# Performance work log

Measured on AMD Instinct MI355X. Metric: run time of the kernel, lower is better.

## Reference

```python
import jax, jax.numpy as jnp
import numpy as np

N = 50000
E = 800000
D = 256
EPS = 1e-5  # BatchNorm eps


def _gcn_conv(x, W, b, row, col):
    # PyG GCNConv: h = x @ W; add self-loops; sym-normalize; scatter-add; + bias
    h = x @ W  # [N, D]
    deg = jnp.zeros((N,), x.dtype).at[col].add(jnp.ones((row.shape[0],), x.dtype))
    dinv = jax.lax.rsqrt(deg)  # deg >= 1 thanks to self-loops
    norm = dinv[row] * dinv[col]  # [E+N]
    msg = h[row] * norm[:, None]  # gather + scale, [E+N, D]
    out = jnp.zeros_like(h).at[col].add(msg)  # scatter-aggregate
    return out + b


def _bn(x, gamma, beta):
    # BatchNorm1d in training mode: batch statistics over nodes
    m = jnp.mean(x, axis=0)
    v = jnp.var(x, axis=0)
    return (x - m) * jax.lax.rsqrt(v + EPS) * gamma + beta


def setup_inputs() -> dict:
    key = jax.random.key(0)
    ks = jax.random.split(key, 4)
    x = jax.random.normal(ks[0], (N, D), dtype=jnp.float32)
    edge_index = jax.random.randint(ks[1], (2, E), 0, N, dtype=jnp.int64)
    s = 1.0 / np.sqrt(D)
    W1 = jax.random.uniform(ks[2], (D, D), jnp.float32, -s, s)
    W2 = jax.random.uniform(ks[3], (D, D), jnp.float32, -s, s)
    z = jnp.zeros((D,), jnp.float32)
    o = jnp.ones((D,), jnp.float32)
    return {"x": x, "edge_index": edge_index,
            "W1": W1, "b1": z, "g1": o, "be1": z,
            "W2": W2, "b2": z, "g2": o, "be2": z}


def reference(x, edge_index, W1, b1, g1, be1, W2, b2, g2, be2):
    loops = jnp.arange(N, dtype=edge_index.dtype)
    row = jnp.concatenate([edge_index[0], loops])  # sources
    col = jnp.concatenate([edge_index[1], loops])  # targets
    # layer 1: GCNConv -> BN -> ReLU (dropout is identity in eval)
    h = _gcn_conv(x, W1, b1, row, col)
    h = jax.nn.relu(_bn(h, g1, be1))
    # layer 2
    h = _gcn_conv(h, W2, b2, row, col)
    h = jax.nn.relu(_bn(h, g2, be2))
    return h
```

## Files before the change

### kernel.cpp

```cpp
#include <hip/hip_runtime.h>
#include <cstdint>
#include <cstddef>

constexpr int N = 50000;
constexpr int E = 800000;
constexpr int D = 256;
constexpr float EPS = 1e-5f;
constexpr int NB = (N + 255) / 256;
constexpr int BN_BLOCKS = 512;
constexpr int GB = (N + 63) / 64;

typedef __attribute__((ext_vector_type(8))) short short8;
typedef __attribute__((ext_vector_type(4))) float f32x4;

__device__ __forceinline__ unsigned short f2bf(float f) {
  union { float f; unsigned u; } c; c.f = f;
  unsigned u = c.u;
  u += 0x7fff + ((u >> 16) & 1);
  return (unsigned short)(u >> 16);
}
__device__ __forceinline__ float bf2f(unsigned short h) {
  union { unsigned u; float f; } c; c.u = ((unsigned)h) << 16;
  return c.f;
}

__global__ void k_detect(const void* __restrict__ ei, int* __restrict__ flag) {
  int t = threadIdx.x;
  const int* p = (const int*)ei;
  int nz = 0;
  for (int i = 2 * t + 1; i < 2048; i += 128) nz |= (p[i] != 0);
  unsigned long long b = __ballot(nz != 0);
  if (t == 0) *flag = (b == 0ULL) ? 1 : 0;
}

__device__ __forceinline__ int edge_at(const void* ei, int is64, long long pos) {
  if (is64) return (int)((const long long*)ei)[pos];
  return ((const int*)ei)[pos];
}

__global__ void k_count(const void* __restrict__ ei, const int* __restrict__ flag,
                        int* __restrict__ degc) {
  int e = blockIdx.x * 256 + threadIdx.x;
  if (e >= E) return;
  int is64 = *flag;
  int c = edge_at(ei, is64, (long long)E + e);
  atomicAdd(&degc[c], 1);
}

__global__ void k_scan_partial(const int* __restrict__ degc, int* __restrict__ bsum,
                               float* __restrict__ dinv) {
  __shared__ int sd[256];
  int t = threadIdx.x;
  int i = blockIdx.x * 256 + t;
  int dv = (i < N) ? degc[i] : 0;
  if (i < N) dinv[i] = rsqrtf((float)(dv + 1));
  int v = (i < N) ? (dv + 1) : 0;
  sd[t] = v;
  __syncthreads();
  for (int s = 128; s > 0; s >>= 1) {
    if (t < s) sd[t] += sd[t + s];
    __syncthreads();
  }
  if (t == 0) bsum[blockIdx.x] = sd[0];
}

__global__ void k_scan_block(int* __restrict__ bsum) {
  __shared__ int sd[256];
  int t = threadIdx.x;
  int v = (t < NB) ? bsum[t] : 0;
  sd[t] = v;
  __syncthreads();
  for (int off = 1; off < 256; off <<= 1) {
    int x = (t >= off) ? sd[t - off] : 0;
    __syncthreads();
    sd[t] += x;
    __syncthreads();
  }
  if (t < NB) bsum[t] = sd[t] - v;
}

__global__ void k_scan_final(const int* __restrict__ degc, const int* __restrict__ bsum,
                             const float* __restrict__ dinv, int* __restrict__ offs,
                             int* __restrict__ curs, int2* __restrict__ epair) {
  __shared__ int sd[256];
  int t = threadIdx.x;
  int i = blockIdx.x * 256 + t;
  int v = (i < N) ? (degc[i] + 1) : 0;
  sd[t] = v;
  __syncthreads();
  for (int off = 1; off < 256; off <<= 1) {
    int x = (t >= off) ? sd[t - off] : 0;
    __syncthreads();
    sd[t] += x;
    __syncthreads();
  }
  if (i < N) {
    int o = bsum[blockIdx.x] + sd[t] - v;
    offs[i] = o;
    curs[i] = o + 1;
    float d = dinv[i];
    epair[o] = make_int2(i, __float_as_int(d * d));
  }
  if (i == N - 1) offs[N] = bsum[blockIdx.x] + sd[t];
}

__global__ void k_fill_edges(const void* __restrict__ ei, const int* __restrict__ flag,
                             const float* __restrict__ dinv, int* __restrict__ curs,
                             int2* __restrict__ epair) {
  int e = blockIdx.x * 256 + threadIdx.x;
  if (e >= E) return;
  int is64 = *flag;
  int r = edge_at(ei, is64, e);
  int c = edge_at(ei, is64, (long long)E + e);
  int p = atomicAdd(&curs[c], 1);
  epair[p] = make_int2(r, __float_as_int(dinv[r] * dinv[c]));
}

__global__ void k_wfrag(const float* __restrict__ W, unsigned short* __restrict__ Wf) {
  int tile = blockIdx.x;
  int lane = threadIdx.x;
  int kstep = tile >> 4, wn = tile & 15;
  int kbase = kstep * 32 + (lane >> 4) * 8;
  int col = wn * 16 + (lane & 15);
  short8 v;
#pragma unroll
  for (int j = 0; j < 8; ++j)
    v[j] = (short)f2bf(W[(size_t)(kbase + j) * 256 + col]);
  *(short8*)&Wf[(((size_t)tile) * 64 + lane) * 8] = v;
}

template <bool A_BF16, bool FUSE_BN>
__global__ __launch_bounds__(256) void k_gemm(const void* __restrict__ Ap,
                                              const unsigned short* __restrict__ Wf,
                                              unsigned short* __restrict__ C,
                                              const float* __restrict__ sc,
                                              const float* __restrict__ sh) {
  __shared__ unsigned short As[64][264];
  int t = threadIdx.x;
  int lane = t & 63;
  int w = t >> 6;
  int row0 = blockIdx.x * 64;
  int l16 = lane & 15, lk = lane >> 4;

  f32x4 acc[4][4];
#pragma unroll
  for (int i = 0; i < 4; ++i)
#pragma unroll
    for (int j = 0; j < 4; ++j) acc[i][j] = (f32x4){0.f, 0.f, 0.f, 0.f};

  int arow = t >> 2;
  int ak0 = (t & 3) * 8;
  int gr = row0 + arow;
  bool inb = (gr < N);

#pragma unroll
  for (int ks = 0; ks < 8; ++ks) {
    int kc = ks * 32 + ak0;
    float f[8] = {0.f, 0.f, 0.f, 0.f, 0.f, 0.f, 0.f, 0.f};
    if (inb) {
      if (A_BF16) {
        const unsigned short* A = (const unsigned short*)Ap;
        short8 v = *(const short8*)&A[(size_t)gr * 256 + kc];
#pragma unroll
        for (int j = 0; j < 8; ++j) f[j] = bf2f((unsigned short)v[j]);
      } else {
        const float* A = (const float*)Ap;
        float4 f0 = *(const float4*)&A[(size_t)gr * 256 + kc];
        float4 f1 = *(const float4*)&A[(size_t)gr * 256 + kc + 4];
        f[0] = f0.x; f[1] = f0.y; f[2] = f0.z; f[3] = f0.w;
        f[4] = f1.x; f[5] = f1.y; f[6] = f1.z; f[7] = f1.w;
      }
    }
    if (FUSE_BN) {
#pragma unroll
      for (int j = 0; j < 8; ++j)
        f[j] = fmaxf(fmaf(f[j], sc[kc + j], sh[kc + j]), 0.f);
    }
    ushort4 u0 = {f2bf(f[0]), f2bf(f[1]), f2bf(f[2]), f2bf(f[3])};
    ushort4 u1 = {f2bf(f[4]), f2bf(f[5]), f2bf(f[6]), f2bf(f[7])};
    *(ushort4*)&As[arow][kc] = u0;
    *(ushort4*)&As[arow][kc + 4] = u1;
  }
  __syncthreads();

#pragma unroll
  for (int ks = 0; ks < 8; ++ks) {
    short8 af[4];
#pragma unroll
    for (int mf = 0; mf < 4; ++mf)
      af[mf] = *(const short8*)&As[mf * 16 + l16][ks * 32 + lk * 8];
#pragma unroll
    for (int nf = 0; nf < 4; ++nf) {
      short8 bf = *(const short8*)&Wf[(((size_t)ks * 16 + w * 4 + nf) * 64 + lane) * 8];
#pragma unroll
      for (int mf = 0; mf < 4; ++mf)
        acc[mf][nf] = __builtin_amdgcn_mfma_f32_16x16x32_bf16(af[mf], bf, acc[mf][nf], 0, 0, 0);
    }
  }
  __syncthreads();

  unsigned short(*Cs)[264] = As;
#pragma unroll
  for (int mf = 0; mf < 4; ++mf)
#pragma unroll
    for (int nf = 0; nf < 4; ++nf)
#pragma unroll
      for (int r = 0; r < 4; ++r)
        Cs[mf * 16 + lk * 4 + r][w * 64 + nf * 16 + l16] = f2bf(acc[mf][nf][r]);
  __syncthreads();
#pragma unroll
  for (int it = 0; it < 8; ++it) {
    int r = it * 8 + (t >> 5);
    int gr2 = row0 + r;
    if (gr2 < N)
      *(short8*)&C[(size_t)gr2 * 256 + (t & 31) * 8] = *(const short8*)&Cs[r][(t & 31) * 8];
  }
}

__global__ __launch_bounds__(256) void k_agg(const unsigned short* __restrict__ h,
                                             const int* __restrict__ offs,
                                             const int2* __restrict__ epair,
                                             const float* __restrict__ bias,
                                             unsigned short* __restrict__ outp) {
  int nd = blockIdx.x * 4 + (threadIdx.x >> 6);
  if (nd >= N) return;
  int node = __builtin_amdgcn_readfirstlane(nd);
  int lane = threadIdx.x & 63;
  int e = offs[node];
  int end = offs[node + 1];
  float a0 = 0.f, a1 = 0.f, a2 = 0.f, a3 = 0.f;

#define ACC4(v, wgt)                                            \
  do {                                                          \
    a0 = fmaf(wgt, bf2f((unsigned short)((v).x & 0xffff)), a0); \
    a1 = fmaf(wgt, bf2f((unsigned short)((v).x >> 16)), a1);    \
    a2 = fmaf(wgt, bf2f((unsigned short)((v).y & 0xffff)), a2); \
    a3 = fmaf(wgt, bf2f((unsigned short)((v).y >> 16)), a3);    \
  } while (0)

  for (; e + 8 <= end; e += 8) {
    int2 p0 = epair[e + 0], p1 = epair[e + 1], p2 = epair[e + 2], p3 = epair[e + 3];
    int2 p4 = epair[e + 4], p5 = epair[e + 5], p6 = epair[e + 6], p7 = epair[e + 7];
    uint2 v0 = *(const uint2*)&h[(size_t)p0.x * 256 + lane * 4];
    uint2 v1 = *(const uint2*)&h[(size_t)p1.x * 256 + lane * 4];
    uint2 v2 = *(const uint2*)&h[(size_t)p2.x * 256 + lane * 4];
    uint2 v3 = *(const uint2*)&h[(size_t)p3.x * 256 + lane * 4];
    uint2 v4 = *(const uint2*)&h[(size_t)p4.x * 256 + lane * 4];
    uint2 v5 = *(const uint2*)&h[(size_t)p5.x * 256 + lane * 4];
    uint2 v6 = *(const uint2*)&h[(size_t)p6.x * 256 + lane * 4];
    uint2 v7 = *(const uint2*)&h[(size_t)p7.x * 256 + lane * 4];
    ACC4(v0, __int_as_float(p0.y));
    ACC4(v1, __int_as_float(p1.y));
    ACC4(v2, __int_as_float(p2.y));
    ACC4(v3, __int_as_float(p3.y));
    ACC4(v4, __int_as_float(p4.y));
    ACC4(v5, __int_as_float(p5.y));
    ACC4(v6, __int_as_float(p6.y));
    ACC4(v7, __int_as_float(p7.y));
  }
  for (; e < end; ++e) {
    int2 p = epair[e];
    uint2 v = *(const uint2*)&h[(size_t)p.x * 256 + lane * 4];
    ACC4(v, __int_as_float(p.y));
  }
#undef ACC4

  float4 bb = ((const float4*)bias)[lane];
  a0 += bb.x; a1 += bb.y; a2 += bb.z; a3 += bb.w;
  ushort4 o = {f2bf(a0), f2bf(a1), f2bf(a2), f2bf(a3)};
  *(ushort4*)&outp[(size_t)nd * 256 + lane * 4] = o;
}

__global__ __launch_bounds__(256) void k_bnpart(const unsigned short* __restrict__ xp,
                                                float* __restrict__ partial) {
  int t = threadIdx.x;
  int lane = t & 63;
  int sub = t >> 6;
  float sx = 0, sy = 0, sz = 0, sw = 0;
  float qx = 0, qy = 0, qz = 0, qw = 0;
  for (int r = blockIdx.x * 4 + sub; r < N; r += gridDim.x * 4) {
    uint2 u = *(const uint2*)&xp[(size_t)r * 256 + lane * 4];
    float vx = bf2f((unsigned short)(u.x & 0xffff));
    float vy = bf2f((unsigned short)(u.x >> 16));
    float vz = bf2f((unsigned short)(u.y & 0xffff));
    float vw = bf2f((unsigned short)(u.y >> 16));
    sx += vx; sy += vy; sz += vz; sw += vw;
    qx = fmaf(vx, vx, qx); qy = fmaf(vy, vy, qy);
    qz = fmaf(vz, vz, qz); qw = fmaf(vw, vw, qw);
  }
  __shared__ float4 ps[256];
  __shared__ float4 pq[256];
  ps[t] = {sx, sy, sz, sw};
  pq[t] = {qx, qy, qz, qw};
  __syncthreads();
  float* pout = partial + (size_t)blockIdx.x * 512;
  if (t < 64) {
    float4 a = ps[t], b = ps[64 + t], c = ps[128 + t], d = ps[192 + t];
    float4 o = {a.x + b.x + c.x + d.x, a.y + b.y + c.y + d.y,
                a.z + b.z + c.z + d.z, a.w + b.w + c.w + d.w};
    ((float4*)pout)[t] = o;
  } else if (t < 128) {
    int l = t - 64;
    float4 a = pq[l], b = pq[64 + l], c = pq[128 + l], d = pq[192 + l];
    float4 o = {a.x + b.x + c.x + d.x, a.y + b.y + c.y + d.y,
                a.z + b.z + c.z + d.z, a.w + b.w + c.w + d.w};
    ((float4*)(pout + 256))[l] = o;
  }
}

__global__ __launch_bounds__(256) void k_bnred(const float* __restrict__ partial,
                                               float* __restrict__ bnsum,
                                               float* __restrict__ bnsq) {
  int t = threadIdx.x;
  float s = 0.f, q = 0.f;
  int b0 = blockIdx.x * (BN_BLOCKS / 16);
  for (int b = b0; b < b0 + BN_BLOCKS / 16; ++b) {
    s += partial[(size_t)b * 512 + t];
    q += partial[(size_t)b * 512 + 256 + t];
  }
  atomicAdd(&bnsum[t], s);
  atomicAdd(&bnsq[t], q);
}

__global__ void k_bnfinal(const float* __restrict__ bnsum, const float* __restrict__ bnsq,
                          const float* __restrict__ g, const float* __restrict__ be,
                          float* __restrict__ sc, float* __restrict__ sh) {
  int t = threadIdx.x;
  const float inv = 1.f / (float)N;
  float m = bnsum[t] * inv;
  float v = bnsq[t] * inv - m * m;
  float s = rsqrtf(v + EPS) * g[t];
  sc[t] = s;
  sh[t] = be[t] - m * s;
}

__global__ __launch_bounds__(256) void k_bnapply(const unsigned short* __restrict__ in,
                                                 float* __restrict__ outp,
                                                 const float* __restrict__ sc,
                                                 const float* __restrict__ sh) {
  int t = threadIdx.x;
  int lane = t & 63;
  int sub = t >> 6;
  float4 s4 = ((const float4*)sc)[lane];
  float4 h4 = ((const float4*)sh)[lane];
  for (int r = blockIdx.x * 4 + sub; r < N; r += gridDim.x * 4) {
    uint2 u = *(const uint2*)&in[(size_t)r * 256 + lane * 4];
    float4 v;
    v.x = fmaxf(fmaf(bf2f((unsigned short)(u.x & 0xffff)), s4.x, h4.x), 0.f);
    v.y = fmaxf(fmaf(bf2f((unsigned short)(u.x >> 16)), s4.y, h4.y), 0.f);
    v.z = fmaxf(fmaf(bf2f((unsigned short)(u.y & 0xffff)), s4.z, h4.z), 0.f);
    v.w = fmaxf(fmaf(bf2f((unsigned short)(u.y >> 16)), s4.w, h4.w), 0.f);
    *(float4*)&outp[(size_t)r * 256 + lane * 4] = v;
  }
}

extern "C" void kernel_launch(void* const* d_in, const int* in_sizes, int n_in,
                              void* d_out, int out_size, void* d_ws, size_t ws_size,
                              hipStream_t stream) {
  const float* x  = (const float*)d_in[0];
  const void*  ei = d_in[1];
  const float* W1 = (const float*)d_in[2];
  const float* b1 = (const float*)d_in[3];
  const float* g1 = (const float*)d_in[4];
  const float* be1 = (const float*)d_in[5];
  const float* W2 = (const float*)d_in[6];
  const float* b2 = (const float*)d_in[7];
  const float* g2 = (const float*)d_in[8];
  const float* be2 = (const float*)d_in[9];
  float* out = (float*)d_out;

  char* base = (char*)d_ws;
  size_t off = 0;
  unsigned short* hbuf = (unsigned short*)(base + off); off += (size_t)N * D * 2;
  unsigned short* abuf = (unsigned short*)(base + off); off += (size_t)N * D * 2;
  unsigned short* Wf1 = (unsigned short*)(base + off);  off += (size_t)D * D * 2;
  unsigned short* Wf2 = (unsigned short*)(base + off);  off += (size_t)D * D * 2;
  int*   degc = (int*)(base + off);   off += (size_t)N * 4;
  float* dinv = (float*)(base + off); off += (size_t)N * 4;
  int*   offs = (int*)(base + off);   off += (size_t)(N + 4) * 4;
  int*   curs = (int*)(base + off);   off += (size_t)N * 4;
  int2*  epair = (int2*)(base + off); off += (size_t)(E + N) * 8;
  float* partial = (float*)(base + off); off += (size_t)BN_BLOCKS * 512 * 4;
  float* bnsum = (float*)(base + off); off += (size_t)D * 4;
  float* bnsq  = (float*)(base + off); off += (size_t)D * 4;
  float* sc1 = (float*)(base + off);  off += (size_t)D * 4;
  float* sh1 = (float*)(base + off);  off += (size_t)D * 4;
  float* sc2 = (float*)(base + off);  off += (size_t)D * 4;
  float* sh2 = (float*)(base + off);  off += (size_t)D * 4;
  int*   bsum = (int*)(base + off);   off += 256 * 4;
  int*   flag = (int*)(base + off);   off += 16;

  k_wfrag<<<128, 64, 0, stream>>>(W1, Wf1);
  k_wfrag<<<128, 64, 0, stream>>>(W2, Wf2);

  hipMemsetAsync(degc, 0, (size_t)N * 4, stream);
  k_detect<<<1, 64, 0, stream>>>(ei, flag);
  k_count<<<(E + 255) / 256, 256, 0, stream>>>(ei, flag, degc);
  k_scan_partial<<<NB, 256, 0, stream>>>(degc, bsum, dinv);
  k_scan_block<<<1, 256, 0, stream>>>(bsum);
  k_scan_final<<<NB, 256, 0, stream>>>(degc, bsum, dinv, offs, curs, epair);
  k_fill_edges<<<(E + 255) / 256, 256, 0, stream>>>(ei, flag, dinv, curs, epair);

  k_gemm<false, false><<<GB, 256, 0, stream>>>(x, Wf1, hbuf, nullptr, nullptr);
  k_agg<<<(N + 3) / 4, 256, 0, stream>>>(hbuf, offs, epair, b1, abuf);
  hipMemsetAsync(bnsum, 0, 2 * (size_t)D * 4, stream);
  k_bnpart<<<BN_BLOCKS, 256, 0, stream>>>(abuf, partial);
  k_bnred<<<16, 256, 0, stream>>>(partial, bnsum, bnsq);
  k_bnfinal<<<1, 256, 0, stream>>>(bnsum, bnsq, g1, be1, sc1, sh1);

  k_gemm<true, true><<<GB, 256, 0, stream>>>(abuf, Wf2, hbuf, sc1, sh1);
  k_agg<<<(N + 3) / 4, 256, 0, stream>>>(hbuf, offs, epair, b2, abuf);
  hipMemsetAsync(bnsum, 0, 2 * (size_t)D * 4, stream);
  k_bnpart<<<BN_BLOCKS, 256, 0, stream>>>(abuf, partial);
  k_bnred<<<16, 256, 0, stream>>>(partial, bnsum, bnsq);
  k_bnfinal<<<1, 256, 0, stream>>>(bnsum, bnsq, g2, be2, sc2, sh2);
  k_bnapply<<<512, 256, 0, stream>>>(abuf, out, sc2, sh2);
}
```

Before: 315.4 us.

## Store features in 32-column panels and split aggregation per panel for cache locality

Intermediate bf16 feature matrices are stored as eight column panels of 32 features, so each panel (about 3.2 MB) can stay resident in cache during the gather. Aggregation is split into 8 chunk blocks per node group, with four lane groups working on different edges and reduced by shuffles. The edge list drops the precomputed weights and stores only source indices, computing dinv[src]*dinv[dst] on the fly. The two weight-fragment launches and the memsets are also merged. The cost is 8x more aggregation blocks, each re-reading offsets and indices, plus smaller 4-byte gathers per lane.

```diff
diff --git a/kernel.cpp b/kernel.cpp
--- a/kernel.cpp
+++ b/kernel.cpp
@@ -9,6 +9,8 @@
 constexpr int NB = (N + 255) / 256;
 constexpr int BN_BLOCKS = 512;
 constexpr int GB = (N + 63) / 64;
+constexpr int PANEL = 32;
+constexpr size_t PSTRIDE = (size_t)N * PANEL;
 
 typedef __attribute__((ext_vector_type(8))) short short8;
 typedef __attribute__((ext_vector_type(4))) float f32x4;
@@ -80,8 +82,8 @@
 }
 
 __global__ void k_scan_final(const int* __restrict__ degc, const int* __restrict__ bsum,
-                             const float* __restrict__ dinv, int* __restrict__ offs,
-                             int* __restrict__ curs, int2* __restrict__ epair) {
+                             int* __restrict__ offs, int* __restrict__ curs,
+                             int* __restrict__ esrc) {
   __shared__ int sd[256];
   int t = threadIdx.x;
   int i = blockIdx.x * 256 + t;
@@ -98,26 +100,28 @@
     int o = bsum[blockIdx.x] + sd[t] - v;
     offs[i] = o;
     curs[i] = o + 1;
-    float d = dinv[i];
-    epair[o] = make_int2(i, __float_as_int(d * d));
+    esrc[o] = i;
   }
   if (i == N - 1) offs[N] = bsum[blockIdx.x] + sd[t];
 }
 
 __global__ void k_fill_edges(const void* __restrict__ ei, const int* __restrict__ flag,
-                             const float* __restrict__ dinv, int* __restrict__ curs,
-                             int2* __restrict__ epair) {
+                             int* __restrict__ curs, int* __restrict__ esrc) {
   int e = blockIdx.x * 256 + threadIdx.x;
   if (e >= E) return;
   int is64 = *flag;
   int r = edge_at(ei, is64, e);
   int c = edge_at(ei, is64, (long long)E + e);
   int p = atomicAdd(&curs[c], 1);
-  epair[p] = make_int2(r, __float_as_int(dinv[r] * dinv[c]));
-}
-
-__global__ void k_wfrag(const float* __restrict__ W, unsigned short* __restrict__ Wf) {
-  int tile = blockIdx.x;
+  esrc[p] = r;
+}
+
+__global__ void k_wfrag(const float* __restrict__ W1, const float* __restrict__ W2,
+                        unsigned short* __restrict__ Wf1, unsigned short* __restrict__ Wf2) {
+  int b = blockIdx.x;
+  const float* W = (b < 128) ? W1 : W2;
+  unsigned short* Wf = (b < 128) ? Wf1 : Wf2;
+  int tile = b & 127;
   int lane = threadIdx.x;
   int kstep = tile >> 4, wn = tile & 15;
   int kbase = kstep * 32 + (lane >> 4) * 8;
@@ -160,7 +164,7 @@
     if (inb) {
       if (A_BF16) {
         const unsigned short* A = (const unsigned short*)Ap;
-        short8 v = *(const short8*)&A[(size_t)gr * 256 + kc];
+        short8 v = *(const short8*)&A[(size_t)ks * PSTRIDE + (size_t)gr * 32 + ak0];
 #pragma unroll
         for (int j = 0; j < 8; ++j) f[j] = bf2f((unsigned short)v[j]);
       } else {
@@ -212,63 +216,68 @@
   for (int it = 0; it < 8; ++it) {
     int r = it * 8 + (t >> 5);
     int gr2 = row0 + r;
+    int cb = t & 31;
+    int ch = cb >> 2;
+    int ic = (cb & 3) * 8;
     if (gr2 < N)
-      *(short8*)&C[(size_t)gr2 * 256 + (t & 31) * 8] = *(const short8*)&Cs[r][(t & 31) * 8];
+      *(short8*)&C[(size_t)ch * PSTRIDE + (size_t)gr2 * 32 + ic] =
+          *(const short8*)&Cs[r][cb * 8];
   }
 }
 
 __global__ __launch_bounds__(256) void k_agg(const unsigned short* __restrict__ h,
                                              const int* __restrict__ offs,
-                                             const int2* __restrict__ epair,
+                                             const int* __restrict__ esrc,
+                                             const float* __restrict__ dinv,
                                              const float* __restrict__ bias,
                                              unsigned short* __restrict__ outp) {
-  int nd = blockIdx.x * 4 + (threadIdx.x >> 6);
+  int bid = blockIdx.x;
+  int chunk = bid & 7;
+  int nd = (bid >> 3) * 4 + (threadIdx.x >> 6);
   if (nd >= N) return;
   int node = __builtin_amdgcn_readfirstlane(nd);
   int lane = threadIdx.x & 63;
+  int g = lane >> 4;
+  int sub = lane & 15;
+  const unsigned short* hp = h + (size_t)chunk * PSTRIDE;
   int e = offs[node];
   int end = offs[node + 1];
-  float a0 = 0.f, a1 = 0.f, a2 = 0.f, a3 = 0.f;
-
-#define ACC4(v, wgt)                                            \
-  do {                                                          \
-    a0 = fmaf(wgt, bf2f((unsigned short)((v).x & 0xffff)), a0); \
-    a1 = fmaf(wgt, bf2f((unsigned short)((v).x >> 16)), a1);    \
-    a2 = fmaf(wgt, bf2f((unsigned short)((v).y & 0xffff)), a2); \
-    a3 = fmaf(wgt, bf2f((unsigned short)((v).y >> 16)), a3);    \
-  } while (0)
+  float dn = dinv[node];
+  float a0 = 0.f, a1 = 0.f;
 
   for (; e + 8 <= end; e += 8) {
-    int2 p0 = epair[e + 0], p1 = epair[e + 1], p2 = epair[e + 2], p3 = epair[e + 3];
-    int2 p4 = epair[e + 4], p5 = epair[e + 5], p6 = epair[e + 6], p7 = epair[e + 7];
-    uint2 v0 = *(const uint2*)&h[(size_t)p0.x * 256 + lane * 4];
-    uint2 v1 = *(const uint2*)&h[(size_t)p1.x * 256 + lane * 4];
-    uint2 v2 = *(const uint2*)&h[(size_t)p2.x * 256 + lane * 4];
-    uint2 v3 = *(const uint2*)&h[(size_t)p3.x * 256 + lane * 4];
-    uint2 v4 = *(const uint2*)&h[(size_t)p4.x * 256 + lane * 4];
-    uint2 v5 = *(const uint2*)&h[(size_t)p5.x * 256 + lane * 4];
-    uint2 v6 = *(const uint2*)&h[(size_t)p6.x * 256 + lane * 4];
-    uint2 v7 = *(const uint2*)&h[(size_t)p7.x * 256 + lane * 4];
-    ACC4(v0, __int_as_float(p0.y));
-    ACC4(v1, __int_as_float(p1.y));
-    ACC4(v2, __int_as_float(p2.y));
-    ACC4(v3, __int_as_float(p3.y));
-    ACC4(v4, __int_as_float(p4.y));
-    ACC4(v5, __int_as_float(p5.y));
-    ACC4(v6, __int_as_float(p6.y));
-    ACC4(v7, __int_as_float(p7.y));
-  }
-  for (; e < end; ++e) {
-    int2 p = epair[e];
-    uint2 v = *(const uint2*)&h[(size_t)p.x * 256 + lane * 4];
-    ACC4(v, __int_as_float(p.y));
-  }
-#undef ACC4
-
-  float4 bb = ((const float4*)bias)[lane];
-  a0 += bb.x; a1 += bb.y; a2 += bb.z; a3 += bb.w;
-  ushort4 o = {f2bf(a0), f2bf(a1), f2bf(a2), f2bf(a3)};
-  *(ushort4*)&outp[(size_t)nd * 256 + lane * 4] = o;
+    int s0 = __builtin_nontemporal_load(&esrc[e + 2 * g]);
+    int s1 = __builtin_nontemporal_load(&esrc[e + 2 * g + 1]);
+    unsigned v0 = *(const unsigned*)&hp[(size_t)s0 * 32 + sub * 2];
+    unsigned v1 = *(const unsigned*)&hp[(size_t)s1 * 32 + sub * 2];
+    float w0 = dinv[s0] * dn;
+    float w1 = dinv[s1] * dn;
+    a0 = fmaf(w0, bf2f((unsigned short)(v0 & 0xffff)), a0);
+    a1 = fmaf(w0, bf2f((unsigned short)(v0 >> 16)), a1);
+    a0 = fmaf(w1, bf2f((unsigned short)(v1 & 0xffff)), a0);
+    a1 = fmaf(w1, bf2f((unsigned short)(v1 >> 16)), a1);
+  }
+  for (; e < end; e += 4) {
+    int idx = e + g;
+    bool act = (idx < end);
+    int s = act ? __builtin_nontemporal_load(&esrc[idx]) : node;
+    float wgt = act ? dinv[s] * dn : 0.f;
+    unsigned v = *(const unsigned*)&hp[(size_t)s * 32 + sub * 2];
+    a0 = fmaf(wgt, bf2f((unsigned short)(v & 0xffff)), a0);
+    a1 = fmaf(wgt, bf2f((unsigned short)(v >> 16)), a1);
+  }
+  a0 += __shfl_xor(a0, 16);
+  a1 += __shfl_xor(a1, 16);
+  a0 += __shfl_xor(a0, 32);
+  a1 += __shfl_xor(a1, 32);
+  if (g == 0) {
+    float2 bb = *(const float2*)&bias[chunk * 32 + sub * 2];
+    unsigned short o0 = f2bf(a0 + bb.x);
+    unsigned short o1 = f2bf(a1 + bb.y);
+    unsigned ov = (unsigned)o0 | ((unsigned)o1 << 16);
+    __builtin_nontemporal_store(
+        ov, (unsigned*)&outp[(size_t)chunk * PSTRIDE + (size_t)nd * 32 + sub * 2]);
+  }
 }
 
 __global__ __launch_bounds__(256) void k_bnpart(const unsigned short* __restrict__ xp,
@@ -276,10 +285,11 @@
   int t = threadIdx.x;
   int lane = t & 63;
   int sub = t >> 6;
+  const unsigned short* base = xp + (size_t)(lane >> 3) * PSTRIDE + (lane & 7) * 4;
   float sx = 0, sy = 0, sz = 0, sw = 0;
   float qx = 0, qy = 0, qz = 0, qw = 0;
   for (int r = blockIdx.x * 4 + sub; r < N; r += gridDim.x * 4) {
-    uint2 u = *(const uint2*)&xp[(size_t)r * 256 + lane * 4];
+    uint2 u = *(const uint2*)&base[(size_t)r * 32];
     float vx = bf2f((unsigned short)(u.x & 0xffff));
     float vy = bf2f((unsigned short)(u.x >> 16));
     float vz = bf2f((unsigned short)(u.y & 0xffff));
@@ -343,8 +353,9 @@
   int sub = t >> 6;
   float4 s4 = ((const float4*)sc)[lane];
   float4 h4 = ((const float4*)sh)[lane];
+  const unsigned short* base = in + (size_t)(lane >> 3) * PSTRIDE + (lane & 7) * 4;
   for (int r = blockIdx.x * 4 + sub; r < N; r += gridDim.x * 4) {
-    uint2 u = *(const uint2*)&in[(size_t)r * 256 + lane * 4];
+    uint2 u = *(const uint2*)&base[(size_t)r * 32];
     float4 v;
     v.x = fmaxf(fmaf(bf2f((unsigned short)(u.x & 0xffff)), s4.x, h4.x), 0.f);
     v.y = fmaxf(fmaf(bf2f((unsigned short)(u.x >> 16)), s4.y, h4.y), 0.f);
@@ -375,14 +386,17 @@
   unsigned short* abuf = (unsigned short*)(base + off); off += (size_t)N * D * 2;
   unsigned short* Wf1 = (unsigned short*)(base + off);  off += (size_t)D * D * 2;
   unsigned short* Wf2 = (unsigned short*)(base + off);  off += (size_t)D * D * 2;
-  int*   degc = (int*)(base + off);   off += (size_t)N * 4;
+  int*   degc = (int*)(base + off);    off += (size_t)N * 4;
+  float* bnsum1 = (float*)(base + off); off += (size_t)D * 4;
+  float* bnsq1  = (float*)(base + off); off += (size_t)D * 4;
+  float* bnsum2 = (float*)(base + off); off += (size_t)D * 4;
+  float* bnsq2  = (float*)(base + off); off += (size_t)D * 4;
+  size_t zero_bytes = (size_t)N * 4 + 4 * (size_t)D * 4;
   float* dinv = (float*)(base + off); off += (size_t)N * 4;
   int*   offs = (int*)(base + off);   off += (size_t)(N + 4) * 4;
   int*   curs = (int*)(base + off);   off += (size_t)N * 4;
-  int2*  epair = (int2*)(base + off); off += (size_t)(E + N) * 8;
+  int*   esrc = (int*)(base + off);   off += (size_t)(E + N) * 4;
   float* partial = (float*)(base + off); off += (size_t)BN_BLOCKS * 512 * 4;
-  float* bnsum = (float*)(base + off); off += (size_t)D * 4;
-  float* bnsq  = (float*)(base + off); off += (size_t)D * 4;
   float* sc1 = (float*)(base + off);  off += (size_t)D * 4;
   float* sh1 = (float*)(base + off);  off += (size_t)D * 4;
   float* sc2 = (float*)(base + off);  off += (size_t)D * 4;
@@ -390,29 +404,29 @@
   int*   bsum = (int*)(base + off);   off += 256 * 4;
   int*   flag = (int*)(base + off);   off += 16;
 
-  k_wfrag<<<128, 64, 0, stream>>>(W1, Wf1);
-  k_wfrag<<<128, 64, 0, stream>>>(W2, Wf2);
-
-  hipMemsetAsync(degc, 0, (size_t)N * 4, stream);
+  hipMemsetAsync(degc, 0, zero_bytes, stream);
+
+  k_wfrag<<<256, 64, 0, stream>>>(W1, W2, Wf1, Wf2);
+
   k_detect<<<1, 64, 0, stream>>>(ei, flag);
   k_count<<<(E + 255) / 256, 256, 0, stream>>>(ei, flag, degc);
   k_scan_partial<<<NB, 256, 0, stream>>>(degc, bsum, dinv);
   k_scan_block<<<1, 256, 0, stream>>>(bsum);
-  k_scan_final<<<NB, 256, 0, stream>>>(degc, bsum, dinv, offs, curs, epair);
-  k_fill_edges<<<(E + 255) / 256, 256, 0, stream>>>(ei, flag, dinv, curs, epair);
+  k_scan_final<<<NB, 256, 0, stream>>>(degc, bsum, offs, curs, esrc);
+  k_fill_edges<<<(E + 255) / 256, 256, 0, stream>>>(ei, flag, curs, esrc);
+
+  int agg_grid = ((N + 3) / 4) * 8;
 
   k_gemm<false, false><<<GB, 256, 0, stream>>>(x, Wf1, hbuf, nullptr, nullptr);
-  k_agg<<<(N + 3) / 4, 256, 0, stream>>>(hbuf, offs, epair, b1, abuf);
-  hipMemsetAsync(bnsum, 0, 2 * (size_t)D * 4, stream);
+  k_agg<<<agg_grid, 256, 0, stream>>>(hbuf, offs, esrc, dinv, b1, abuf);
   k_bnpart<<<BN_BLOCKS, 256, 0, stream>>>(abuf, partial);
-  k_bnred<<<16, 256, 0, stream>>>(partial, bnsum, bnsq);
-  k_bnfinal<<<1, 256, 0, stream>>>(bnsum, bnsq, g1, be1, sc1, sh1);
+  k_bnred<<<16, 256, 0, stream>>>(partial, bnsum1, bnsq1);
+  k_bnfinal<<<1, 256, 0, stream>>>(bnsum1, bnsq1, g1, be1, sc1, sh1);
 
   k_gemm<true, true><<<GB, 256, 0, stream>>>(abuf, Wf2, hbuf, sc1, sh1);
-  k_agg<<<(N + 3) / 4, 256, 0, stream>>>(hbuf, offs, epair, b2, abuf);
-  hipMemsetAsync(bnsum, 0, 2 * (size_t)D * 4, stream);
+  k_agg<<<agg_grid, 256, 0, stream>>>(hbuf, offs, esrc, dinv, b2, abuf);
   k_bnpart<<<BN_BLOCKS, 256, 0, stream>>>(abuf, partial);
-  k_bnred<<<16, 256, 0, stream>>>(partial, bnsum, bnsq);
-  k_bnfinal<<<1, 256, 0, stream>>>(bnsum, bnsq, g2, be2, sc2, sh2);
+  k_bnred<<<16, 256, 0, stream>>>(partial, bnsum2, bnsq2);
+  k_bnfinal<<<1, 256, 0, stream>>>(bnsum2, bnsq2, g2, be2, sc2, sh2);
   k_bnapply<<<512, 256, 0, stream>>>(abuf, out, sc2, sh2);
 }
```

After: 557.5 us. 1.77x slower.
